# Performance work log

Hardware: AMD Instinct MI355X
Metric: run time of the kernel (lower is better)

Reference implementation:

```python
import jax, jax.numpy as jnp
import numpy as np

# dims
B, N, D = 2, 4096, 384
NUM_HEADS, KEY_DIM, VALUE_DIM = 8, 48, 48
TOP_K = 128
IDX_HEADS, IDX_DIM = 2, 32
SCALE = KEY_DIM ** (-0.5)


def setup_inputs() -> dict:
    key = jax.random.key(0)
    ks = jax.random.split(key, 9)
    def xavier(k, shape):
        fan_in, fan_out = shape[0], shape[1]
        lim = (6.0 / (fan_in + fan_out)) ** 0.5
        return jax.random.uniform(k, shape, jnp.float32, -lim, lim)
    return {
        "x": jax.random.normal(ks[0], (B, N, D), jnp.float32),
        # lightning indexer params
        "wq_idx": xavier(ks[1], (D, IDX_HEADS * IDX_DIM)),
        "wk_idx": xavier(ks[2], (D, IDX_DIM)),
        "ww_idx": xavier(ks[3], (D, IDX_HEADS)),
        # attention params (stored as (in, out) for x @ W)
        "wq": xavier(ks[4], (D, NUM_HEADS * KEY_DIM)),
        "wk": xavier(ks[5], (D, KEY_DIM)),
        "wv": xavier(ks[6], (D, VALUE_DIM)),
        "wo": xavier(ks[7], (NUM_HEADS * VALUE_DIM, D)),
    }


def _forward(x, wq_idx, wk_idx, ww_idx, wq, wk, wv, wo):
    b, n, d = x.shape
    # ---- Lightning indexer: I[q,s] = sum_h w[q,h] * relu(qi[q,h] . ki[s]) ----
    qi = (x @ wq_idx).reshape(b, n, IDX_HEADS, IDX_DIM)      # (B,N,Hi,dki)
    ki = x @ wk_idx                                           # (B,N,dki)
    w_idx = x @ ww_idx                                        # (B,N,Hi)
    raw = jax.nn.relu(jnp.einsum('bqhd,bsd->bqhs', qi, ki))   # (B,Nq,Hi,Nk)
    index_scores = jnp.einsum('bqhs,bqh->bqs', raw, w_idx)    # (B,Nq,Nk)

    # ---- MQA projections ----
    q = (x @ wq).reshape(b, n, NUM_HEADS, KEY_DIM).transpose(0, 2, 1, 3)  # (B,H,N,dk)
    k = x @ wk                                                # (B,N,dk) single KV head
    v = x @ wv                                                # (B,N,dv)

    # ---- top-k select + gather ----
    kk = min(TOP_K, n)
    _, top_idx = jax.lax.top_k(index_scores, kk)              # (B,Nq,k)
    bidx = jnp.arange(b)[:, None, None]
    sel_k = k[bidx, top_idx]                                  # (B,Nq,k,dk)
    sel_v = v[bidx, top_idx]                                  # (B,Nq,k,dv)

    # ---- sparse attention over selected keys ----
    attn = jnp.einsum('bhqd,bqkd->bhqk', q, sel_k) * SCALE    # (B,H,Nq,k)
    probs = jax.nn.softmax(attn, axis=-1)
    out = jnp.einsum('bhqk,bqkd->bhqd', probs, sel_v)         # (B,H,Nq,dv)
    out = out.transpose(0, 2, 1, 3).reshape(b, n, NUM_HEADS * VALUE_DIM)
    return out @ wo                                           # (B,N,D)


def reference(x, wq_idx, wk_idx, ww_idx, wq, wk, wv, wo):
    return _forward(x, wq_idx, wk_idx, ww_idx, wq, wk, wv, wo)
```

## Files before the change

### kernel.cpp

```cpp
#include <hip/hip_runtime.h>
#include <math.h>

#define NB 2
#define NSEQ 4096
#define DMODEL 384
#define NH 8
#define DKQ 48
#define DV 48
#define TOPK 128
#define NQ (NB*NSEQ)

#define QKV_COLS 480
#define C_Q 0
#define C_K 384
#define C_V 432
#define IDX_COLS 128
#define P_QI 0
#define P_KI 64
#define P_W  96
#define ATT_SCALE 0.14433756729740643f

typedef double v4d  __attribute__((ext_vector_type(4)));
typedef float  f32x4 __attribute__((ext_vector_type(4)));
typedef short  s16x8 __attribute__((ext_vector_type(8)));

__device__ inline void bsplit(float v, unsigned short& h, unsigned short& l) {
    unsigned hb = __float_as_uint(v);
    unsigned short hi = (unsigned short)((hb + 0x7FFFu + ((hb >> 16) & 1u)) >> 16);
    float hf = __uint_as_float(((unsigned)hi) << 16);
    float r = v - hf;
    unsigned rb = __float_as_uint(r);
    unsigned short lo = (unsigned short)((rb + 0x7FFFu + ((rb >> 16) & 1u)) >> 16);
    h = hi; l = lo;
}

__global__ void k_split(const float* __restrict__ x,
                        unsigned short* __restrict__ xhi, unsigned short* __restrict__ xlo) {
    int i = blockIdx.x * 256 + threadIdx.x;
    if (i < NQ * DMODEL) {
        unsigned short h, l;
        bsplit(x[i], h, l);
        xhi[i] = h; xlo[i] = l;
    }
}

__global__ void k_concat(const float* __restrict__ wq_idx, const float* __restrict__ wk_idx,
                         const float* __restrict__ ww_idx, const float* __restrict__ wq,
                         const float* __restrict__ wk, const float* __restrict__ wv,
                         const float* __restrict__ wo,
                         unsigned short* __restrict__ WqT_hi, unsigned short* __restrict__ WqT_lo,
                         unsigned short* __restrict__ WoT_hi, unsigned short* __restrict__ WoT_lo,
                         float* __restrict__ Wi_cat) {
    int i = blockIdx.x * 256 + threadIdx.x;
    const int NQK = QKV_COLS * DMODEL;
    const int NWO = DMODEL * DMODEL;
    if (i < NQK) {
        int n = i / DMODEL, k = i % DMODEL;
        float v;
        if (n < 384)      v = wq[(size_t)k*384 + n];
        else if (n < 432) v = wk[(size_t)k*48 + (n-384)];
        else              v = wv[(size_t)k*48 + (n-432)];
        unsigned short h, l; bsplit(v, h, l);
        WqT_hi[i] = h; WqT_lo[i] = l;
    } else if (i < NQK + NWO) {
        int j = i - NQK;
        int n = j / DMODEL, k = j % DMODEL;
        float v = wo[(size_t)k*384 + n];
        unsigned short h, l; bsplit(v, h, l);
        WoT_hi[j] = h; WoT_lo[j] = l;
    } else if (i < NQK + NWO + DMODEL*IDX_COLS) {
        int j = i - NQK - NWO;
        int d = j / IDX_COLS, c = j % IDX_COLS;
        float v;
        if (c < 64)       v = wq_idx[d*64 + c];
        else if (c < 96)  v = wk_idx[d*32 + (c-64)];
        else if (c < 98)  v = ww_idx[d*2 + (c-96)];
        else              v = 0.f;
        Wi_cat[j] = v;
    }
}

#define GLDK 40
__global__ __launch_bounds__(256) void k_gemm_mfma(
        const unsigned short* __restrict__ Ahi, const unsigned short* __restrict__ Alo,
        const unsigned short* __restrict__ Bhi, const unsigned short* __restrict__ Blo,
        float* __restrict__ C, int N, int ldc) {
    __shared__ unsigned short At[2][128][GLDK];
    __shared__ unsigned short Bt[2][64][GLDK];
    const int t = threadIdx.x;
    const int lane = t & 63, wid = t >> 6;
    const int row0 = blockIdx.y * 128, col0 = blockIdx.x * 64;
    const int ml = lane & 15, kq = lane >> 4;
    const int wm = (wid & 1) * 64, wn = (wid >> 1) * 32;

    unsigned short mv = (unsigned short)(__float_as_uint((float)(ml + 1)) >> 16);
    unsigned short one = 0x3F80;
    s16x8 pa, pb;
    #pragma unroll
    for (int j = 0; j < 8; j++) { pa[j] = (short)mv; pb[j] = (short)one; }
    f32x4 zf = (f32x4){0.f, 0.f, 0.f, 0.f};
    f32x4 rowp = __builtin_amdgcn_mfma_f32_16x16x32_bf16(pa, pb, zf, 0, 0, 0);
    f32x4 colp = __builtin_amdgcn_mfma_f32_16x16x32_bf16(pb, pa, zf, 0, 0, 0);
    int rowm[4], colm[4];
    #pragma unroll
    for (int r = 0; r < 4; r++) {
        rowm[r] = (((int)(rowp[r] * 0.03125f + 0.5f)) - 1) & 15;
        colm[r] = (((int)(colp[r] * 0.03125f + 0.5f)) - 1) & 15;
    }

    f32x4 acc[4][2];
    #pragma unroll
    for (int mt = 0; mt < 4; mt++)
        #pragma unroll
        for (int nt = 0; nt < 2; nt++) acc[mt][nt] = zf;

    for (int k0 = 0; k0 < DMODEL; k0 += 32) {
        #pragma unroll
        for (int i = 0; i < 4; i++) {
            int ch = t + 256*i;
            int arr = ch >> 9, rem = ch & 511;
            int r = rem >> 2, p = rem & 3;
            const unsigned short* src = arr ? Alo : Ahi;
            *(int4*)&At[arr][r][p*8] = *(const int4*)(src + (size_t)(row0 + r)*DMODEL + k0 + p*8);
        }
        #pragma unroll
        for (int i = 0; i < 2; i++) {
            int ch = t + 256*i;
            int arr = ch >> 8, rem = ch & 255;
            int r = rem >> 2, p = rem & 3;
            const unsigned short* src = arr ? Blo : Bhi;
            int gc = col0 + r;
            int4 v = {0, 0, 0, 0};
            if (gc < N) v = *(const int4*)(src + (size_t)gc*DMODEL + k0 + p*8);
            *(int4*)&Bt[arr][r][p*8] = v;
        }
        __syncthreads();
        s16x8 af[4][2], bfr[2][2];
        #pragma unroll
        for (int mt = 0; mt < 4; mt++)
            #pragma unroll
            for (int h = 0; h < 2; h++)
                af[mt][h] = *(const s16x8*)&At[h][wm + mt*16 + ml][kq*8];
        #pragma unroll
        for (int nt = 0; nt < 2; nt++)
            #pragma unroll
            for (int h = 0; h < 2; h++)
                bfr[nt][h] = *(const s16x8*)&Bt[h][wn + nt*16 + ml][kq*8];
        #pragma unroll
        for (int mt = 0; mt < 4; mt++)
            #pragma unroll
            for (int nt = 0; nt < 2; nt++) {
                acc[mt][nt] = __builtin_amdgcn_mfma_f32_16x16x32_bf16(af[mt][0], bfr[nt][0], acc[mt][nt], 0, 0, 0);
                acc[mt][nt] = __builtin_amdgcn_mfma_f32_16x16x32_bf16(af[mt][0], bfr[nt][1], acc[mt][nt], 0, 0, 0);
                acc[mt][nt] = __builtin_amdgcn_mfma_f32_16x16x32_bf16(af[mt][1], bfr[nt][0], acc[mt][nt], 0, 0, 0);
            }
        __syncthreads();
    }
    #pragma unroll
    for (int mt = 0; mt < 4; mt++)
        #pragma unroll
        for (int nt = 0; nt < 2; nt++)
            #pragma unroll
            for (int r = 0; r < 4; r++) {
                int rr = row0 + wm + mt*16 + rowm[r];
                int cc = col0 + wn + nt*16 + colm[r];
                if (cc < N) C[(size_t)rr*ldc + cc] = acc[mt][nt][r];
            }
}

__global__ __launch_bounds__(256) void k_proj64(const float* __restrict__ A,
                                                const float* __restrict__ W,
                                                double* __restrict__ P) {
    __shared__ float At[16][32];
    __shared__ float Bt[16][IDX_COLS];
    const int t  = threadIdx.x;
    const int tx = t & 15;
    const int ty = t >> 4;
    const int row0 = blockIdx.x * 32;
    double acc[2][8] = {};

    for (int k0 = 0; k0 < DMODEL; k0 += 16) {
        if (t < 128) {
            int m = t >> 2, kc = t & 3;
            float4 a = *(const float4*)(A + (size_t)(row0 + m)*DMODEL + k0 + kc*4);
            At[kc*4+0][m] = a.x; At[kc*4+1][m] = a.y;
            At[kc*4+2][m] = a.z; At[kc*4+3][m] = a.w;
        }
        for (int i = 0; i < 2; i++) {
            int lin = t + i*256;
            int kk = lin >> 5, c4 = lin & 31;
            float4 b = *(const float4*)(W + (size_t)(k0+kk)*IDX_COLS + c4*4);
            *(float4*)&Bt[kk][c4*4] = b;
        }
        __syncthreads();
        for (int kk = 0; kk < 16; kk++) {
            float a2[2], b8[8];
            a2[0] = At[kk][ty*2]; a2[1] = At[kk][ty*2+1];
            *(float4*)&b8[0] = *(const float4*)&Bt[kk][tx*8];
            *(float4*)&b8[4] = *(const float4*)&Bt[kk][tx*8+4];
            for (int i = 0; i < 2; i++)
                for (int j = 0; j < 8; j++)
                    acc[i][j] += (double)a2[i] * (double)b8[j];
        }
        __syncthreads();
    }
    for (int i = 0; i < 2; i++)
        for (int j = 0; j < 8; j++)
            P[(size_t)(row0 + ty*2 + i)*IDX_COLS + tx*8 + j] = acc[i][j];
}

__global__ __launch_bounds__(256) void k_score_mfma(const double* __restrict__ P,
                                                    unsigned int* __restrict__ K32,
                                                    int qstart) {
    __shared__ double A0[32][33];
    __shared__ double A1[32][33];
    __shared__ double Bk[32][129];
    __shared__ double wsh[2][32];
    const int t = threadIdx.x;
    const int lane = t & 63;
    const int wid = t >> 6;
    const int g0 = qstart + blockIdx.y * 32;
    const int b  = g0 / NSEQ;
    const int s0 = blockIdx.x * 128;

    for (int i = 0; i < 8; i++) {
        int lin = t + i*256;
        int q = lin >> 6, c = lin & 63;
        double v = P[(size_t)(g0 + q)*IDX_COLS + P_QI + c];
        if (c < 32) A0[c][q] = v; else A1[c-32][q] = v;
    }
    for (int i = 0; i < 16; i++) {
        int lin = t + i*256;
        int s = lin >> 5, c = lin & 31;
        Bk[c][s] = P[(size_t)(b*NSEQ + s0 + s)*IDX_COLS + P_KI + c];
    }
    if (t < 64) wsh[t & 1][t >> 1] = P[(size_t)(g0 + (t >> 1))*IDX_COLS + P_W + (t & 1)];

    const int qw = (wid & 1) * 16;
    const int sw = (wid >> 1) * 64;
    const int ml = lane & 15;
    const int kl = lane >> 4;

    v4d zero = (v4d){0.0, 0.0, 0.0, 0.0};
    v4d rowp = __builtin_amdgcn_mfma_f64_16x16x4f64((double)(ml+1), 1.0, zero, 0, 0, 0);
    v4d colp = __builtin_amdgcn_mfma_f64_16x16x4f64(1.0, (double)(ml+1), zero, 0, 0, 0);
    int rowm[4], colm[4];
    #pragma unroll
    for (int r = 0; r < 4; r++) {
        rowm[r] = (((int)(rowp[r] * 0.25 + 0.5)) - 1) & 15;
        colm[r] = (((int)(colp[r] * 0.25 + 0.5)) - 1) & 15;
    }

    __syncthreads();

    v4d acc0[4], acc1[4];
    #pragma unroll
    for (int st = 0; st < 4; st++) { acc0[st] = zero; acc1[st] = zero; }

    #pragma unroll
    for (int k4 = 0; k4 < 8; k4++) {
        int k = k4*4 + kl;
        double a0 = A0[k][qw + ml];
        double a1 = A1[k][qw + ml];
        #pragma unroll
        for (int st = 0; st < 4; st++) {
            double bb = Bk[k][sw + st*16 + ml];
            acc0[st] = __builtin_amdgcn_mfma_f64_16x16x4f64(a0, bb, acc0[st], 0, 0, 0);
            acc1[st] = __builtin_amdgcn_mfma_f64_16x16x4f64(a1, bb, acc1[st], 0, 0, 0);
        }
    }

    #pragma unroll
    for (int reg = 0; reg < 4; reg++) {
        int q = qw + rowm[reg];
        double w0 = wsh[0][q], w1 = wsh[1][q];
        #pragma unroll
        for (int st = 0; st < 4; st++) {
            double sc = w0 * fmax(acc0[st][reg], 0.0) + w1 * fmax(acc1[st][reg], 0.0);
            size_t oidx = (size_t)(blockIdx.y*32 + q)*NSEQ + s0 + sw + st*16 + colm[reg];
            float sf = (float)sc;
            unsigned int ub = __float_as_uint(sf);
            unsigned int u = (ub & 0x80000000u) ? ~ub : (ub | 0x80000000u);
            __builtin_nontemporal_store(u, &K32[oidx]);
        }
    }
}

__global__ __launch_bounds__(256) void k_topk(const unsigned int* __restrict__ K32,
                                              int* __restrict__ IDX, int qstart) {
    __shared__ unsigned int pool[1024];
    __shared__ unsigned int wred[4];
    __shared__ unsigned int s_b, s_need, s_flag, s_cnt, s_n;
    unsigned int* CK = pool;
    int* CI = (int*)(pool + 512);
    const int t = threadIdx.x, lane = t & 63;
    const int wid = t >> 6;
    const int q = blockIdx.x;
    const unsigned int* krow = K32 + (size_t)q * NSEQ;
    int* orow = IDX + (size_t)(qstart + q) * TOPK;

    unsigned int kr[16];
    #pragma unroll
    for (int jj = 0; jj < 4; jj++) {
        uint4 v = *(const uint4*)(krow + (t*4 + 1024*jj));
        kr[jj*4+0] = v.x; kr[jj*4+1] = v.y; kr[jj*4+2] = v.z; kr[jj*4+3] = v.w;
    }
    unsigned int mymax = kr[0];
    #pragma unroll
    for (int j = 1; j < 16; j++) mymax = kr[j] > mymax ? kr[j] : mymax;
    const unsigned int p16 = mymax >> 16;

    unsigned int Tw = 0;
    #pragma unroll
    for (int bit = 15; bit >= 0; --bit) {
        unsigned int trial = Tw | (1u << bit);
        if (__popcll(__ballot(p16 >= trial)) >= 32) Tw = trial;
    }
    if (lane == 0) wred[wid] = Tw;
    if (t == 0) { s_cnt = 0; s_n = 0; s_need = TOPK; s_flag = 0; }
    __syncthreads();
    unsigned int T16 = wred[0];
    T16 = wred[1] < T16 ? wred[1] : T16;
    T16 = wred[2] < T16 ? wred[2] : T16;
    T16 = wred[3] < T16 ? wred[3] : T16;

    #pragma unroll
    for (int j = 0; j < 16; j++) {
        if ((kr[j] >> 16) >= T16) {
            unsigned int pos = atomicAdd(&s_n, 1u);
            if (pos < 512u) { CK[pos] = kr[j]; CI[pos] = (j >> 2)*1024 + t*4 + (j & 3); }
        }
    }
    __syncthreads();
    const unsigned int n = s_n;

    if (n <= 512u) {
        if (wid == 0) {
            unsigned int ck[8]; int ci[8]; bool cv[8];
            #pragma unroll
            for (int e = 0; e < 8; e++) {
                int id = lane + e*64;
                cv[e] = (unsigned int)id < n;
                ck[e] = cv[e] ? CK[id] : 0u;
                ci[e] = cv[e] ? CI[id] : 0;
            }
            unsigned int T = 0;
            for (int bit = 31; bit >= 0; --bit) {
                unsigned int trial = T | (1u << bit);
                unsigned int c = 0;
                #pragma unroll
                for (int e = 0; e < 8; e++)
                    c += (unsigned int)__popcll(__ballot(cv[e] && ck[e] >= trial));
                if (c >= (unsigned int)TOPK) T = trial;
            }
            unsigned int G = 0, E = 0;
            #pragma unroll
            for (int e = 0; e < 8; e++) {
                G += (unsigned int)__popcll(__ballot(cv[e] && ck[e] > T));
                E += (unsigned int)__popcll(__ballot(cv[e] && ck[e] == T));
            }
            const unsigned int need = (unsigned int)TOPK - G;
            const unsigned long long ltm = (1ull << lane) - 1ull;

            unsigned int cbase = 0;
            #pragma unroll
            for (int e = 0; e < 8; e++) {
                bool em = cv[e] && ck[e] > T;
                unsigned long long m = __ballot(em);
                if (em) orow[cbase + __popcll(m & ltm)] = ci[e];
                cbase += (unsigned int)__popcll(m);
            }
            if (E == need) {
                #pragma unroll
                for (int e = 0; e < 8; e++) {
                    bool em = cv[e] && ck[e] == T;
                    unsigned long long m = __ballot(em);
                    if (em) orow[cbase + __popcll(m & ltm)] = ci[e];
                    cbase += (unsigned int)__popcll(m);
                }
            } else {
                unsigned int r = 0;
                for (int bit = 11; bit >= 0; --bit) {
                    unsigned int trial = r | (1u << bit);
                    unsigned int c = 0;
                    #pragma unroll
                    for (int e = 0; e < 8; e++)
                        c += (unsigned int)__popcll(__ballot(cv[e] && ck[e] == T &&
                                 (unsigned int)ci[e] <= trial));
                    if (c <= need) r = trial;
                }
                #pragma unroll
                for (int e = 0; e < 8; e++) {
                    bool em = cv[e] && ck[e] == T && (unsigned int)ci[e] <= r;
                    unsigned long long m = __ballot(em);
                    if (em) orow[cbase + __popcll(m & ltm)] = ci[e];
                    cbase += (unsigned int)__popcll(m);
                }
            }
        }
        return;
    }

    unsigned int amask = 0;
    #pragma unroll
    for (int j = 0; j < 16; j++)
        if ((kr[j] >> 16) >= T16) amask |= (1u << j);

    unsigned int (*hist)[256] = (unsigned int (*)[256])pool;
    auto clearhist = [&]() {
        #pragma unroll
        for (int w = 0; w < 4; w++) hist[w][t] = 0;
        __syncthreads();
    };
    auto decide = [&]() {
        if (wid == 0) {
            unsigned int c[4];
            #pragma unroll
            for (int k2 = 0; k2 < 4; k2++)
                c[k2] = hist[0][lane*4+k2] + hist[1][lane*4+k2]
                      + hist[2][lane*4+k2] + hist[3][lane*4+k2];
            unsigned int run = c[0] + c[1] + c[2] + c[3];
            #pragma unroll
            for (int d2 = 1; d2 < 64; d2 <<= 1) {
                unsigned int v = __shfl_down(run, d2, 64);
                if (lane + d2 < 64) run += v;
            }
            unsigned int need = s_need;
            unsigned int Sb[5];
            Sb[0] = run; Sb[1] = run - c[0]; Sb[2] = Sb[1] - c[1];
            Sb[3] = Sb[2] - c[2]; Sb[4] = Sb[3] - c[3];
            #pragma unroll
            for (int j = 0; j < 4; j++) {
                if (Sb[j] >= need && Sb[j+1] < need) {
                    s_b = (unsigned int)(lane*4 + j);
                    s_need = need - Sb[j+1];
                    s_flag = (need - Sb[j+1] == c[j]) ? 1u : 0u;
                }
            }
        }
        __syncthreads();
    };

    #pragma unroll 1
    for (int level = 0; level < 4; ++level) {
        const int sh = 24 - 8*level;
        clearhist();
        #pragma unroll
        for (int j = 0; j < 16; j++) {
            if ((amask >> j) & 1u)
                atomicAdd(&hist[wid][(kr[j] >> sh) & 255u], 1u);
        }
        __syncthreads();
        decide();
        const unsigned int bstar = s_b;

        if (s_flag) {
            #pragma unroll
            for (int j = 0; j < 16; j++) {
                if (((amask >> j) & 1u) && (((kr[j] >> sh) & 255u) >= bstar))
                    orow[atomicAdd(&s_cnt, 1u)] = (j >> 2)*1024 + t*4 + (j & 3);
            }
            return;
        }
        unsigned int nm = 0;
        #pragma unroll
        for (int j = 0; j < 16; j++) {
            if ((amask >> j) & 1u) {
                unsigned int d = (kr[j] >> sh) & 255u;
                if (d > bstar) orow[atomicAdd(&s_cnt, 1u)] = (j >> 2)*1024 + t*4 + (j & 3);
                else if (d == bstar) nm |= (1u << j);
            }
        }
        amask = nm;
    }

    const unsigned int needF = s_need;
    unsigned int base = 0;
    #pragma unroll 1
    for (int jj = 0; jj < 4; jj++) {
        unsigned int m4 = (amask >> (jj*4)) & 0xFu;
        unsigned int cnt = __popc(m4);
        unsigned int inc = cnt;
        #pragma unroll
        for (int d2 = 1; d2 < 64; d2 <<= 1) {
            unsigned int v = __shfl_up(inc, d2, 64);
            if (lane >= d2) inc += v;
        }
        if (lane == 63) wred[wid] = inc;
        __syncthreads();
        unsigned int woff = 0;
        for (int w2 = 0; w2 < wid; w2++) woff += wred[w2];
        unsigned int T = wred[0] + wred[1] + wred[2] + wred[3];
        unsigned int p = base + woff + inc - cnt;
        #pragma unroll
        for (int c = 0; c < 4; c++) {
            if ((m4 >> c) & 1u) {
                if (p < needF) orow[atomicAdd(&s_cnt, 1u)] = jj*1024 + t*4 + c;
                p++;
            }
        }
        base += T;
        __syncthreads();
    }
}

__global__ __launch_bounds__(512) void k_attn(const float* __restrict__ Y,
                                              const int* __restrict__ IDX,
                                              unsigned short* __restrict__ ctx_hi,
                                              unsigned short* __restrict__ ctx_lo) {
    __shared__ float Ksw[TOPK][64];
    __shared__ float Vt[DV * TOPK];
    __shared__ float qsh[NH*DKQ];
    __shared__ float prs[NH*TOPK];
    __shared__ int   idxs[TOPK];
    const int g = blockIdx.x;
    const int b = g / NSEQ;
    const int t = threadIdx.x;
    const int lane = t & 63, wid = t >> 6;

    if (t < TOPK) idxs[t] = IDX[(size_t)g*TOPK + t];
    if (t < NH*DKQ) qsh[t] = Y[(size_t)g*QKV_COLS + C_Q + t];
    __syncthreads();
    #pragma unroll
    for (int i = 0; i < 6; i++) {
        int e = t + 512*i;
        int j = e / 24, p = e % 24;
        const float* src = Y + (size_t)(b*NSEQ + idxs[j])*QKV_COLS + C_K;
        float4 v = *(const float4*)(src + p*4);
        if (p < 12) {
            *(float4*)&Ksw[j][(p ^ (j & 7)) * 4] = v;
        } else {
            int dd0 = (p - 12) * 4;
            #pragma unroll
            for (int c = 0; c < 4; c++) {
                int dd = dd0 + c;
                Vt[dd*TOPK + (((j >> 2) ^ (dd & 31)) << 2) + (j & 3)] = ((const float*)&v)[c];
            }
        }
    }
    __syncthreads();

    float4 qf[12];
    #pragma unroll
    for (int c = 0; c < 12; c++) qf[c] = *(const float4*)&qsh[wid*DKQ + c*4];
    float lo0 = 0.f, lo1 = 0.f;
    const int sw = (lane & 7);
    #pragma unroll
    for (int c = 0; c < 12; c++) {
        float4 k0 = *(const float4*)&Ksw[lane][(c ^ sw) * 4];
        float4 k1 = *(const float4*)&Ksw[lane + 64][(c ^ sw) * 4];
        float4 qv = qf[c];
        lo0 += qv.x*k0.x + qv.y*k0.y + qv.z*k0.z + qv.w*k0.w;
        lo1 += qv.x*k1.x + qv.y*k1.y + qv.z*k1.z + qv.w*k1.w;
    }
    lo0 *= ATT_SCALE; lo1 *= ATT_SCALE;
    float m = fmaxf(lo0, lo1);
    #pragma unroll
    for (int d = 32; d >= 1; d >>= 1) m = fmaxf(m, __shfl_xor(m, d, 64));
    float e0 = __expf(lo0 - m), e1 = __expf(lo1 - m);
    float sum = e0 + e1;
    #pragma unroll
    for (int d = 32; d >= 1; d >>= 1) sum += __shfl_xor(sum, d, 64);
    float inv = 1.0f / sum;
    prs[wid*TOPK + lane]      = e0 * inv;
    prs[wid*TOPK + lane + 64] = e1 * inv;
    __syncthreads();

    if (lane < DV) {
        const int dd = lane;
        const int dsw = dd & 31;
        float acc = 0.f;
        #pragma unroll
        for (int jb = 0; jb < 32; jb++) {
            float4 pv = *(const float4*)&prs[wid*TOPK + jb*4];
            float4 vt = *(const float4*)&Vt[dd*TOPK + ((jb ^ dsw) << 2)];
            acc += pv.x*vt.x + pv.y*vt.y + pv.z*vt.z + pv.w*vt.w;
        }
        unsigned short ch, cl;
        bsplit(acc, ch, cl);
        ctx_hi[(size_t)g*(NH*DV) + wid*DV + dd] = ch;
        ctx_lo[(size_t)g*(NH*DV) + wid*DV + dd] = cl;
    }
}

extern "C" void kernel_launch(void* const* d_in, const int* in_sizes, int n_in,
                              void* d_out, int out_size, void* d_ws, size_t ws_size,
                              hipStream_t stream) {
    const float* x      = (const float*)d_in[0];
    const float* wq_idx = (const float*)d_in[1];
    const float* wk_idx = (const float*)d_in[2];
    const float* ww_idx = (const float*)d_in[3];
    const float* wq     = (const float*)d_in[4];
    const float* wk     = (const float*)d_in[5];
    const float* wv     = (const float*)d_in[6];
    const float* wo     = (const float*)d_in[7];
    float* out = (float*)d_out;
    char*  ws  = (char*)d_ws;

    size_t off = 0;
    auto carve = [&](size_t bytes) { size_t o = off; off = (off + bytes + 255) & ~(size_t)255; return o; };
    size_t oWqh = carve((size_t)QKV_COLS*DMODEL*2);
    size_t oWql = carve((size_t)QKV_COLS*DMODEL*2);
    size_t oWoh = carve((size_t)DMODEL*DMODEL*2);
    size_t oWol = carve((size_t)DMODEL*DMODEL*2);
    size_t oWi  = carve((size_t)DMODEL*IDX_COLS*4);
    size_t oXh  = carve((size_t)NQ*DMODEL*2);
    size_t oXl  = carve((size_t)NQ*DMODEL*2);
    size_t oY   = carve((size_t)NQ*QKV_COLS*4);
    size_t oP   = carve((size_t)NQ*IDX_COLS*8);
    size_t oIdx = carve((size_t)NQ*TOPK*4);
    size_t oCh  = carve((size_t)NQ*NH*DV*2);
    size_t oCl  = carve((size_t)NQ*NH*DV*2);
    size_t oKL  = off;

    int QC = NQ;
    while (QC > 32 && oKL + (size_t)QC*NSEQ*4 > ws_size) QC >>= 1;

    unsigned short* WqT_hi = (unsigned short*)(ws + oWqh);
    unsigned short* WqT_lo = (unsigned short*)(ws + oWql);
    unsigned short* WoT_hi = (unsigned short*)(ws + oWoh);
    unsigned short* WoT_lo = (unsigned short*)(ws + oWol);
    float*  Wi_cat = (float*)(ws + oWi);
    unsigned short* xhi = (unsigned short*)(ws + oXh);
    unsigned short* xlo = (unsigned short*)(ws + oXl);
    float*  Y      = (float*)(ws + oY);
    double* P      = (double*)(ws + oP);
    int*    IDX    = (int*)(ws + oIdx);
    unsigned short* ctx_hi = (unsigned short*)(ws + oCh);
    unsigned short* ctx_lo = (unsigned short*)(ws + oCl);
    unsigned int* K32 = (unsigned int*)(ws + oKL);

    int ncat = QKV_COLS*DMODEL + DMODEL*DMODEL + DMODEL*IDX_COLS;
    k_split<<<(NQ*DMODEL + 255)/256, 256, 0, stream>>>(x, xhi, xlo);
    k_concat<<<(ncat + 255)/256, 256, 0, stream>>>(wq_idx, wk_idx, ww_idx, wq, wk, wv, wo,
                                                   WqT_hi, WqT_lo, WoT_hi, WoT_lo, Wi_cat);
    k_gemm_mfma<<<dim3((QKV_COLS + 63)/64, NQ/128), 256, 0, stream>>>(xhi, xlo, WqT_hi, WqT_lo, Y, QKV_COLS, QKV_COLS);
    k_proj64<<<NQ/32, 256, 0, stream>>>(x, Wi_cat, P);
    for (int qs = 0; qs < NQ; qs += QC) {
        k_score_mfma<<<dim3(NSEQ/128, QC/32), 256, 0, stream>>>(P, K32, qs);
        k_topk<<<QC, 256, 0, stream>>>(K32, IDX, qs);
    }
    k_attn<<<NQ, 512, 0, stream>>>(Y, IDX, ctx_hi, ctx_lo);
    k_gemm_mfma<<<dim3(DMODEL/64, NQ/128), 256, 0, stream>>>(ctx_hi, ctx_lo, WoT_hi, WoT_lo, out, DMODEL, DMODEL);
}
```

Measured before the change: 473.3 us.

## Compute attention PV via per-lane products and shuffle reduction instead of transposed V

```diff
diff --git a/kernel.cpp b/kernel.cpp
--- a/kernel.cpp
+++ b/kernel.cpp
@@ -281,7 +281,7 @@
             float sf = (float)sc;
             unsigned int ub = __float_as_uint(sf);
             unsigned int u = (ub & 0x80000000u) ? ~ub : (ub | 0x80000000u);
-            __builtin_nontemporal_store(u, &K32[oidx]);
+            K32[oidx] = u;
         }
     }
 }
@@ -504,14 +504,15 @@
     }
 }
 
+#define VPAD 52
 __global__ __launch_bounds__(512) void k_attn(const float* __restrict__ Y,
                                               const int* __restrict__ IDX,
                                               unsigned short* __restrict__ ctx_hi,
                                               unsigned short* __restrict__ ctx_lo) {
     __shared__ float Ksw[TOPK][64];
-    __shared__ float Vt[DV * TOPK];
+    __shared__ float Vs[TOPK][VPAD];
     __shared__ float qsh[NH*DKQ];
-    __shared__ float prs[NH*TOPK];
+    __shared__ float red[NH][4][VPAD];
     __shared__ int   idxs[TOPK];
     const int g = blockIdx.x;
     const int b = g / NSEQ;
@@ -527,16 +528,8 @@
         int j = e / 24, p = e % 24;
         const float* src = Y + (size_t)(b*NSEQ + idxs[j])*QKV_COLS + C_K;
         float4 v = *(const float4*)(src + p*4);
-        if (p < 12) {
-            *(float4*)&Ksw[j][(p ^ (j & 7)) * 4] = v;
-        } else {
-            int dd0 = (p - 12) * 4;
-            #pragma unroll
-            for (int c = 0; c < 4; c++) {
-                int dd = dd0 + c;
-                Vt[dd*TOPK + (((j >> 2) ^ (dd & 31)) << 2) + (j & 3)] = ((const float*)&v)[c];
-            }
-        }
+        if (p < 12) *(float4*)&Ksw[j][(p ^ (j & 7)) * 4] = v;
+        else        *(float4*)&Vs[j][(p - 12) * 4] = v;
     }
     __syncthreads();
 
@@ -562,24 +555,39 @@
     #pragma unroll
     for (int d = 32; d >= 1; d >>= 1) sum += __shfl_xor(sum, d, 64);
     float inv = 1.0f / sum;
-    prs[wid*TOPK + lane]      = e0 * inv;
-    prs[wid*TOPK + lane + 64] = e1 * inv;
+    const float p0 = e0 * inv, p1 = e1 * inv;
+
+    float acc[48];
+    #pragma unroll
+    for (int c = 0; c < 12; c++) {
+        float4 v0 = *(const float4*)&Vs[lane][c*4];
+        float4 v1 = *(const float4*)&Vs[lane + 64][c*4];
+        acc[c*4+0] = p0*v0.x + p1*v1.x;
+        acc[c*4+1] = p0*v0.y + p1*v1.y;
+        acc[c*4+2] = p0*v0.z + p1*v1.z;
+        acc[c*4+3] = p0*v0.w + p1*v1.w;
+    }
+    #pragma unroll
+    for (int d = 1; d <= 8; d <<= 1)
+        #pragma unroll
+        for (int c = 0; c < 48; c++)
+            acc[c] += __shfl_xor(acc[c], d, 64);
+    if ((lane & 15) == 0) {
+        const int grp = lane >> 4;
+        #pragma unroll
+        for (int c = 0; c < 12; c++) {
+            float4 tmp = {acc[c*4+0], acc[c*4+1], acc[c*4+2], acc[c*4+3]};
+            *(float4*)&red[wid][grp][c*4] = tmp;
+        }
+    }
     __syncthreads();
-
     if (lane < DV) {
-        const int dd = lane;
-        const int dsw = dd & 31;
-        float acc = 0.f;
-        #pragma unroll
-        for (int jb = 0; jb < 32; jb++) {
-            float4 pv = *(const float4*)&prs[wid*TOPK + jb*4];
-            float4 vt = *(const float4*)&Vt[dd*TOPK + ((jb ^ dsw) << 2)];
-            acc += pv.x*vt.x + pv.y*vt.y + pv.z*vt.z + pv.w*vt.w;
-        }
+        float s = red[wid][0][lane] + red[wid][1][lane]
+                + red[wid][2][lane] + red[wid][3][lane];
         unsigned short ch, cl;
-        bsplit(acc, ch, cl);
-        ctx_hi[(size_t)g*(NH*DV) + wid*DV + dd] = ch;
-        ctx_lo[(size_t)g*(NH*DV) + wid*DV + dd] = cl;
+        bsplit(s, ch, cl);
+        ctx_hi[(size_t)g*(NH*DV) + wid*DV + lane] = ch;
+        ctx_lo[(size_t)g*(NH*DV) + wid*DV + lane] = cl;
     }
 }
 
```

Result: slower. 567.8 us (+20.0%).
